# Performance work log

Measured on AMD Instinct MI355X. Metric: run time of the kernel, lower is better.

The kernel has to match this reference:

```python
import jax, jax.numpy as jnp
import numpy as np

MARGIN = 0.1
SEMIHARD = True


def setup_inputs() -> dict:
    key = jax.random.key(0)
    k1, k2 = jax.random.split(key)
    N, D = 512, 128
    embeddings = jax.random.normal(k1, (N, D), dtype=jnp.float32)
    labels = jax.random.randint(k2, (N,), 0, 64, dtype=jnp.int64)
    return {"embeddings": embeddings, "labels": labels}


def _triplet_mask(labels):
    # mask[a, p, n] True iff a,p,n distinct, labels[a]==labels[p], labels[a]!=labels[n]
    n = labels.shape[0]
    ine = ~jnp.eye(n, dtype=bool)                       # [N, N] i != j
    distinct = ine[:, :, None] & ine[:, None, :] & ine[None, :, :]
    leq = labels[None, :] == labels[:, None]            # [N, N] label equality
    valid = leq[:, :, None] & ~leq[:, None, :]
    return distinct & valid


def reference(embeddings, labels):
    # L2-normalize rows, cosine similarity matrix
    norms = jnp.linalg.norm(embeddings, ord=2, axis=1, keepdims=True)
    e = embeddings / norms
    all_sim = e @ e.T                                   # [N, N]
    mask = _triplet_mask(labels).astype(all_sim.dtype)  # [N, N, N]
    # loss[a,p,n] = relu(-sim[a,p] + sim[a,n] + margin) * mask
    anc_pos = all_sim[:, :, None]                       # [N, N, 1]
    anc_neg = all_sim[:, None, :]                       # [N, 1, N]
    loss = jax.nn.relu(anc_neg - anc_pos + MARGIN) * mask
    if SEMIHARD:
        num_active = jnp.sum((loss > 1e-16).astype(loss.dtype))
        return jnp.sum(loss) / (num_active + 1e-16)
    else:
        return jnp.sum(loss) / jnp.sum(mask)
```

## Files before the change

### kernel.cpp

```cpp
#include <hip/hip_runtime.h>
#include <math.h>

#define MARGIN 0.1f
#define NN 512
#define DD 128
#define NT 256
#define AB 2
#define TROWS 64
#define NTILES (NN / TROWS)
#define NBLK (NN / AB)
#define MAXPOS 256

__global__ __launch_bounds__(NT) void triplet_partial_kernel(
        const float* __restrict__ emb, const int* __restrict__ labels,
        double* __restrict__ part_sum, int* __restrict__ part_cnt) {
    __shared__ int   lab[NN];
    __shared__ __align__(16) float ea[AB][DD];
    __shared__ __align__(16) float tile[TROWS * DD];
    __shared__ float simr[AB][NN];
    __shared__ int   pos[AB][MAXPOS];
    __shared__ int   npos[AB];
    __shared__ double red_s[NT / 64];
    __shared__ int    red_c[NT / 64];

    const int b  = blockIdx.x;
    const int t  = threadIdx.x;
    const int a0 = b * AB;
    const int jj = t >> 2;
    const int ks = t & 3;

    for (int j = t; j < NN; j += NT) lab[j] = labels[j];
    {
        int ai = t >> 7;
        int k  = t & 127;
        ea[ai][k] = emb[(size_t)(a0 + ai) * DD + k];
    }
    if (t < AB) npos[t] = 0;
    __syncthreads();

    float inva[AB];
    #pragma unroll
    for (int ai = 0; ai < AB; ++ai) {
        float s = 0.f;
        for (int k = 0; k < DD; ++k) { float v = ea[ai][k]; s += v * v; }
        inva[ai] = 1.0f / sqrtf(s);
    }

    float w0[32], w1[32];
    #pragma unroll
    for (int i = 0; i < 32; ++i) {
        w0[i] = ea[0][ks * 32 + i];
        w1[i] = ea[1][ks * 32 + i];
    }

    const float4* __restrict__ emb4 = reinterpret_cast<const float4*>(emb);
    float4* tile4 = reinterpret_cast<float4*>(tile);

    for (int tl = 0; tl < NTILES; ++tl) {
        const int rbase = tl * TROWS;
        __syncthreads();
        #pragma unroll
        for (int it = 0; it < 8; ++it) {
            int c   = t + NT * it;
            int row = c >> 5;
            int c4  = c & 31;
            float4 v = emb4[(size_t)(rbase + row) * 32 + c4];
            tile4[row * 32 + (c4 ^ (row & 7))] = v;
        }
        __syncthreads();

        float d0 = 0.f, d1 = 0.f, nsq = 0.f;
        #pragma unroll
        for (int i2 = 0; i2 < 8; ++i2) {
            float4 v = tile4[jj * 32 + ((ks * 8 + i2) ^ (jj & 7))];
            int ib = i2 * 4;
            d0  += v.x * w0[ib] + v.y * w0[ib + 1] + v.z * w0[ib + 2] + v.w * w0[ib + 3];
            d1  += v.x * w1[ib] + v.y * w1[ib + 1] + v.z * w1[ib + 2] + v.w * w1[ib + 3];
            nsq += v.x * v.x + v.y * v.y + v.z * v.z + v.w * v.w;
        }
        d0  += __shfl_xor(d0, 1, 64);  d0  += __shfl_xor(d0, 2, 64);
        d1  += __shfl_xor(d1, 1, 64);  d1  += __shfl_xor(d1, 2, 64);
        nsq += __shfl_xor(nsq, 1, 64); nsq += __shfl_xor(nsq, 2, 64);
        if (ks == 0) {
            float rn = 1.0f / sqrtf(nsq);
            int j = rbase + jj;
            simr[0][j] = d0 * inva[0] * rn;
            simr[1][j] = d1 * inva[1] * rn;
        }
    }
    __syncthreads();

    for (int j = t; j < NN; j += NT) {
        #pragma unroll
        for (int ai = 0; ai < AB; ++ai) {
            if (j != a0 + ai && lab[j] == lab[a0 + ai]) {
                int idx = atomicAdd(&npos[ai], 1);
                if (idx < MAXPOS) pos[ai][idx] = j;
            }
        }
    }
    __syncthreads();

    double lsum = 0.0;
    int    lcnt = 0;
    #pragma unroll
    for (int ai = 0; ai < AB; ++ai) {
        const int la = lab[a0 + ai];
        const int np = min(npos[ai], MAXPOS);
        for (int pi = 0; pi < np; ++pi) {
            const float sap = simr[ai][pos[ai][pi]];
            for (int n = t; n < NN; n += NT) {
                if (lab[n] != la) {
                    float d = simr[ai][n] - sap + MARGIN;
                    if (d > 0.f)    lsum += (double)d;
                    if (d > 1e-16f) lcnt += 1;
                }
            }
        }
    }

    for (int off = 32; off > 0; off >>= 1) {
        lsum += __shfl_down(lsum, off, 64);
        lcnt += __shfl_down(lcnt, off, 64);
    }
    const int wid = t >> 6, lane = t & 63;
    if (lane == 0) { red_s[wid] = lsum; red_c[wid] = lcnt; }
    __syncthreads();
    if (t == 0) {
        double s = 0.0; int c = 0;
        for (int w = 0; w < NT / 64; ++w) { s += red_s[w]; c += red_c[w]; }
        part_sum[b] = s;
        part_cnt[b] = c;
    }
}

__global__ __launch_bounds__(NBLK) void finalize_kernel(
        const double* __restrict__ part_sum, const int* __restrict__ part_cnt,
        float* __restrict__ out) {
    __shared__ double rs[NBLK / 64];
    __shared__ int    rc[NBLK / 64];
    const int t = threadIdx.x;
    double s = part_sum[t];
    int    c = part_cnt[t];
    for (int off = 32; off > 0; off >>= 1) {
        s += __shfl_down(s, off, 64);
        c += __shfl_down(c, off, 64);
    }
    const int wid = t >> 6, lane = t & 63;
    if (lane == 0) { rs[wid] = s; rc[wid] = c; }
    __syncthreads();
    if (t == 0) {
        double S = 0.0; int C = 0;
        for (int w = 0; w < NBLK / 64; ++w) { S += rs[w]; C += rc[w]; }
        out[0] = (float)(S / ((double)C + 1e-16));
    }
}

extern "C" void kernel_launch(void* const* d_in, const int* in_sizes, int n_in,
                              void* d_out, int out_size, void* d_ws, size_t ws_size,
                              hipStream_t stream) {
    const float* emb  = (const float*)d_in[0];
    const int* labels = (const int*)d_in[1];

    double* part_sum = (double*)d_ws;
    int*    part_cnt = (int*)((char*)d_ws + NBLK * sizeof(double));
    float*  out      = (float*)d_out;

    triplet_partial_kernel<<<NBLK, NT, 0, stream>>>(emb, labels, part_sum, part_cnt);
    finalize_kernel<<<1, NBLK, 0, stream>>>(part_sum, part_cnt, out);
}
```

Measured before the change: 75.43 us.

## Double-buffer embedding tiles with register prefetch and parallelize anchor norm

Embedding tiles are now double-buffered in shared memory. The next tile's global loads are issued into registers before the current tile's dot products run, so memory latency overlaps with compute, and one barrier per tile is dropped. Separately, the serial 128-element anchor-norm loop run by every thread is replaced by per-thread partial sums over the cached weights, combined with a shuffle reduction. This doubles tile shared-memory use (to about 64KB) and adds register pressure from the 8 float4 prefetch registers, which could lower occupancy.

After: 85.68 us. 1.14x slower.

```diff
diff --git a/kernel.cpp b/kernel.cpp
--- a/kernel.cpp
+++ b/kernel.cpp
@@ -16,7 +16,7 @@
         double* __restrict__ part_sum, int* __restrict__ part_cnt) {
     __shared__ int   lab[NN];
     __shared__ __align__(16) float ea[AB][DD];
-    __shared__ __align__(16) float tile[TROWS * DD];
+    __shared__ __align__(16) float tile[2][TROWS * DD];
     __shared__ float simr[AB][NN];
     __shared__ int   pos[AB][MAXPOS];
     __shared__ int   npos[AB];
@@ -29,6 +29,17 @@
     const int jj = t >> 2;
     const int ks = t & 3;
 
+    const float4* __restrict__ emb4 = reinterpret_cast<const float4*>(emb);
+
+    float4 ld[8];
+    #pragma unroll
+    for (int it = 0; it < 8; ++it) {
+        int c   = t + NT * it;
+        int row = c >> 5;
+        int c4  = c & 31;
+        ld[it] = emb4[(size_t)row * 32 + c4];
+    }
+
     for (int j = t; j < NN; j += NT) lab[j] = labels[j];
     {
         int ai = t >> 7;
@@ -38,14 +49,6 @@
     if (t < AB) npos[t] = 0;
     __syncthreads();
 
-    float inva[AB];
-    #pragma unroll
-    for (int ai = 0; ai < AB; ++ai) {
-        float s = 0.f;
-        for (int k = 0; k < DD; ++k) { float v = ea[ai][k]; s += v * v; }
-        inva[ai] = 1.0f / sqrtf(s);
-    }
-
     float w0[32], w1[32];
     #pragma unroll
     for (int i = 0; i < 32; ++i) {
@@ -53,26 +56,43 @@
         w1[i] = ea[1][ks * 32 + i];
     }
 
-    const float4* __restrict__ emb4 = reinterpret_cast<const float4*>(emb);
-    float4* tile4 = reinterpret_cast<float4*>(tile);
+    float nsq0 = 0.f, nsq1 = 0.f;
+    #pragma unroll
+    for (int i = 0; i < 32; ++i) {
+        nsq0 += w0[i] * w0[i];
+        nsq1 += w1[i] * w1[i];
+    }
+    nsq0 += __shfl_xor(nsq0, 1, 64); nsq0 += __shfl_xor(nsq0, 2, 64);
+    nsq1 += __shfl_xor(nsq1, 1, 64); nsq1 += __shfl_xor(nsq1, 2, 64);
+    const float inva0 = 1.0f / sqrtf(nsq0);
+    const float inva1 = 1.0f / sqrtf(nsq1);
 
     for (int tl = 0; tl < NTILES; ++tl) {
-        const int rbase = tl * TROWS;
-        __syncthreads();
+        float4* tb = reinterpret_cast<float4*>(tile[tl & 1]);
         #pragma unroll
         for (int it = 0; it < 8; ++it) {
             int c   = t + NT * it;
             int row = c >> 5;
             int c4  = c & 31;
-            float4 v = emb4[(size_t)(rbase + row) * 32 + c4];
-            tile4[row * 32 + (c4 ^ (row & 7))] = v;
+            tb[row * 32 + (c4 ^ (row & 7))] = ld[it];
         }
         __syncthreads();
+
+        if (tl + 1 < NTILES) {
+            const int rb = (tl + 1) * TROWS;
+            #pragma unroll
+            for (int it = 0; it < 8; ++it) {
+                int c   = t + NT * it;
+                int row = c >> 5;
+                int c4  = c & 31;
+                ld[it] = emb4[(size_t)(rb + row) * 32 + c4];
+            }
+        }
 
         float d0 = 0.f, d1 = 0.f, nsq = 0.f;
         #pragma unroll
         for (int i2 = 0; i2 < 8; ++i2) {
-            float4 v = tile4[jj * 32 + ((ks * 8 + i2) ^ (jj & 7))];
+            float4 v = tb[jj * 32 + ((ks * 8 + i2) ^ (jj & 7))];
             int ib = i2 * 4;
             d0  += v.x * w0[ib] + v.y * w0[ib + 1] + v.z * w0[ib + 2] + v.w * w0[ib + 3];
             d1  += v.x * w1[ib] + v.y * w1[ib + 1] + v.z * w1[ib + 2] + v.w * w1[ib + 3];
@@ -83,9 +103,9 @@
         nsq += __shfl_xor(nsq, 1, 64); nsq += __shfl_xor(nsq, 2, 64);
         if (ks == 0) {
             float rn = 1.0f / sqrtf(nsq);
-            int j = rbase + jj;
-            simr[0][j] = d0 * inva[0] * rn;
-            simr[1][j] = d1 * inva[1] * rn;
+            int j = tl * TROWS + jj;
+            simr[0][j] = d0 * inva0 * rn;
+            simr[1][j] = d1 * inva1 * rn;
         }
     }
     __syncthreads();
```
